# Performance work log

Measured on AMD Instinct MI355X. Metric: run time of the kernel, lower is better.

The kernel has to match this reference:

```python
import jax, jax.numpy as jnp
import numpy as np

STATE_DIM = 256
LATENT_DIM = 64
HIDDEN = 64
NUM_EMB = 2048
BATCH = 32768


def setup_inputs() -> dict:
    key = jax.random.key(0)
    ks = jax.random.split(key, 10)
    s = lambda *sh: 1.0 / np.sqrt(sh[0])
    return {
        "x": jax.random.normal(ks[0], (BATCH, STATE_DIM), dtype=jnp.float32),
        # encoder: Linear(state_dim, 64) -> ReLU -> Linear(64, latent_dim)
        "enc_w1": jax.random.uniform(ks[1], (STATE_DIM, HIDDEN), jnp.float32, -s(STATE_DIM), s(STATE_DIM)),
        "enc_b1": jax.random.uniform(ks[2], (HIDDEN,), jnp.float32, -s(STATE_DIM), s(STATE_DIM)),
        "enc_w2": jax.random.uniform(ks[3], (HIDDEN, LATENT_DIM), jnp.float32, -s(HIDDEN), s(HIDDEN)),
        "enc_b2": jax.random.uniform(ks[4], (LATENT_DIM,), jnp.float32, -s(HIDDEN), s(HIDDEN)),
        # codebook
        "emb": jax.random.normal(ks[5], (NUM_EMB, LATENT_DIM), dtype=jnp.float32),
        # decoder: Linear(latent_dim, 64) -> ReLU -> Linear(64, state_dim)
        "dec_w1": jax.random.uniform(ks[6], (LATENT_DIM, HIDDEN), jnp.float32, -s(LATENT_DIM), s(LATENT_DIM)),
        "dec_b1": jax.random.uniform(ks[7], (HIDDEN,), jnp.float32, -s(LATENT_DIM), s(LATENT_DIM)),
        "dec_w2": jax.random.uniform(ks[8], (HIDDEN, STATE_DIM), jnp.float32, -s(HIDDEN), s(HIDDEN)),
        "dec_b2": jax.random.uniform(ks[9], (STATE_DIM,), jnp.float32, -s(HIDDEN), s(HIDDEN)),
    }


def reference(x, enc_w1, enc_b1, enc_w2, enc_b2, emb, dec_w1, dec_b1, dec_w2, dec_b2):
    # encoder MLP: z_e [B, latent]
    h = jax.nn.relu(x @ enc_w1 + enc_b1)
    z_e = h @ enc_w2 + enc_b2
    # squared euclidean distances to codebook, expanded form: [B, K]
    # ||z - e||^2 = ||z||^2 - 2 z.e + ||e||^2  (same argmin as broadcast form)
    d = (jnp.sum(z_e * z_e, axis=1, keepdims=True)
         - 2.0 * (z_e @ emb.T)
         + jnp.sum(emb * emb, axis=1)[None, :])
    z_q_idx = jnp.argmin(d, axis=1)           # [B]
    z_q = emb[z_q_idx]                        # [B, latent]
    # decoder MLP
    hd = jax.nn.relu(z_q @ dec_w1 + dec_b1)
    x_recon = hd @ dec_w2 + dec_b2
    return (x_recon, z_e, z_q)
```

## Files before the change

### kernel.cpp

```cpp
#include <hip/hip_runtime.h>

#define BATCH   32768
#define SD      256
#define LD      64
#define HDIM    64
#define NEMB    2048
#define REFINE_THR_Q 5e-4f

typedef short  short8 __attribute__((ext_vector_type(8)));
typedef float  f32x4  __attribute__((ext_vector_type(4)));

__device__ __forceinline__ unsigned short f2bf(float f) {
    unsigned int u = __float_as_uint(f);
    u = (u + 0x7FFFu + ((u >> 16) & 1u)) >> 16;
    return (unsigned short)u;
}
__device__ __forceinline__ float bf2f(unsigned short h) {
    return __uint_as_float(((unsigned int)h) << 16);
}

__global__ __launch_bounds__(256) void k0_all(const float* __restrict__ emb,
                                              const float* __restrict__ dw1,
                                              const float* __restrict__ dw2,
                                              const float* __restrict__ ew1,
                                              const float* __restrict__ ew2,
                                              float* __restrict__ e2q,
                                              unsigned short* __restrict__ eh,
                                              unsigned short* __restrict__ el,
                                              unsigned short* __restrict__ w1h,
                                              unsigned short* __restrict__ w1l,
                                              unsigned short* __restrict__ w2h,
                                              unsigned short* __restrict__ w2l,
                                              unsigned short* __restrict__ w1eh,
                                              unsigned short* __restrict__ w1em,
                                              unsigned short* __restrict__ w1el,
                                              unsigned short* __restrict__ w2eh,
                                              unsigned short* __restrict__ w2em,
                                              unsigned short* __restrict__ w2el,
                                              int* __restrict__ count) {
    int b = blockIdx.x;
    int t = threadIdx.x;
    if (b < 8) {
        int k = b * 256 + t;
        if (k == 0) *count = 0;
        const float* er = emb + (size_t)k * LD;
        unsigned short hrow[LD], lrow[LD];
        float s = 0.f;
#pragma unroll
        for (int q = 0; q < LD; ++q) {
            float v = er[q];
            s += v * v;
            unsigned short h = f2bf(v);
            hrow[q] = h;
            lrow[q] = f2bf(v - bf2f(h));
        }
        e2q[k] = -0.5f * s;
        short8* dh = (short8*)(eh + (size_t)k * LD);
        short8* dl = (short8*)(el + (size_t)k * LD);
#pragma unroll
        for (int q = 0; q < 8; ++q) {
            dh[q] = *(short8*)&hrow[q * 8];
            dl[q] = *(short8*)&lrow[q * 8];
        }
    } else if (b < 24) {
        int e = (b - 8) * 256 + t;
        int j = e >> 6, k = e & 63;
        float v = dw1[k * HDIM + j];
        unsigned short h = f2bf(v);
        w1h[e] = h; w1l[e] = f2bf(v - bf2f(h));
    } else if (b < 88) {
        int e = (b - 24) * 256 + t;
        int j = e >> 6, k = e & 63;
        float v = dw2[k * SD + j];
        unsigned short h = f2bf(v);
        w2h[e] = h; w2l[e] = f2bf(v - bf2f(h));
    } else if (b < 152) {
        int e = (b - 88) * 256 + t;
        int kt = e >> 11, j = (e & 2047) >> 5, kk = e & 31;
        int k = kt * 32 + kk;
        float v = ew1[k * HDIM + j];
        unsigned short h = f2bf(v);
        float r1 = v - bf2f(h);
        unsigned short m = f2bf(r1);
        float r2 = r1 - bf2f(m);
        w1eh[e] = h; w1em[e] = m; w1el[e] = f2bf(r2);
    } else {
        int e = (b - 152) * 256 + t;
        int kt = e >> 11, j = (e & 2047) >> 5, kk = e & 31;
        int k = kt * 32 + kk;
        float v = ew2[k * LD + j];
        unsigned short h = f2bf(v);
        float r1 = v - bf2f(h);
        unsigned short m = f2bf(r1);
        float r2 = r1 - bf2f(m);
        w2eh[e] = h; w2em[e] = m; w2el[e] = f2bf(r2);
    }
}

#define MF(Afr, Bfr, C) __builtin_amdgcn_mfma_f32_16x16x32_bf16(Afr, Bfr, C, 0, 0, 0)

#define E_WLOAD(P, KT, JT) do {                                             \
    size_t wo_ = (size_t)(KT) * 2048 + ((JT) * 16 + lo) * 32 + hi * 8;      \
    P##h = *(const short8*)(w1eh + wo_);                                    \
    P##m = *(const short8*)(w1em + wo_);                                    \
    P##l = *(const short8*)(w1el + wo_);                                    \
} while (0)

#define E_COMP(P, JT) do {                                                  \
    f32x4 c_ = c1[JT];                                                      \
    c_ = MF(xl8, P##h, c_);                                                 \
    c_ = MF(xm8, P##m, c_);                                                 \
    c_ = MF(xh8, P##l, c_);                                                 \
    c_ = MF(xm8, P##h, c_);                                                 \
    c_ = MF(xh8, P##m, c_);                                                 \
    c_ = MF(xh8, P##h, c_);                                                 \
    c1[JT] = c_;                                                            \
} while (0)

#define K2_LOAD(P, t) do {                                                  \
    const unsigned short* ph_ = ehp + (size_t)(t) * 16 * LD;                \
    const unsigned short* pl_ = elp + (size_t)(t) * 16 * LD;                \
    P##a0 = *(const short8*)(ph_);                                          \
    P##a1 = *(const short8*)(ph_ + 32);                                     \
    P##a2 = *(const short8*)(pl_);                                          \
    P##a3 = *(const short8*)(pl_ + 32);                                     \
    P##e2 = *(const f32x4*)(e2q + cbase + (t) * 16 + hi * 4);               \
} while (0)

#define K2_COMP(P, t) do {                                                  \
    f32x4 acc_[4];                                                          \
    _Pragma("unroll")                                                       \
    for (int g = 0; g < 4; ++g) {                                           \
        f32x4 c_;                                                           \
        c_ = __builtin_amdgcn_mfma_f32_16x16x32_bf16(P##a0, bh[g][0], P##e2, 0, 0, 0); \
        c_ = __builtin_amdgcn_mfma_f32_16x16x32_bf16(P##a1, bh[g][1], c_, 0, 0, 0);    \
        c_ = __builtin_amdgcn_mfma_f32_16x16x32_bf16(P##a2, bh[g][0], c_, 0, 0, 0);    \
        c_ = __builtin_amdgcn_mfma_f32_16x16x32_bf16(P##a3, bh[g][1], c_, 0, 0, 0);    \
        c_ = __builtin_amdgcn_mfma_f32_16x16x32_bf16(P##a0, bl[g][0], c_, 0, 0, 0);    \
        c_ = __builtin_amdgcn_mfma_f32_16x16x32_bf16(P##a1, bl[g][1], c_, 0, 0, 0);    \
        acc_[g] = c_;                                                       \
    }                                                                       \
    _Pragma("unroll")                                                       \
    for (int g = 0; g < 4; ++g) {                                           \
        float m_ = fmaxf(fmaxf(acc_[g][0], acc_[g][1]),                     \
                         fmaxf(acc_[g][2], acc_[g][3]));                    \
        bool win_ = (m_ > bb[g]);                                           \
        qv[g] = win_ ? acc_[g] : qv[g];                                     \
        tt[g] = win_ ? (t) : tt[g];                                         \
        b2v[g] = fmaxf(b2v[g], fminf(bb[g], m_));                           \
        bb[g] = fmaxf(bb[g], m_);                                           \
    }                                                                       \
} while (0)

__global__ __launch_bounds__(256, 2) void k_fused(const float* __restrict__ x,
                                                  const unsigned short* __restrict__ w1eh,
                                                  const unsigned short* __restrict__ w1em,
                                                  const unsigned short* __restrict__ w1el,
                                                  const float* __restrict__ b1,
                                                  const unsigned short* __restrict__ w2eh,
                                                  const unsigned short* __restrict__ w2em,
                                                  const unsigned short* __restrict__ w2el,
                                                  const float* __restrict__ b2,
                                                  const unsigned short* __restrict__ eh,
                                                  const unsigned short* __restrict__ el,
                                                  const float* __restrict__ e2q,
                                                  float* __restrict__ zOut,
                                                  int* __restrict__ idx,
                                                  int* __restrict__ list,
                                                  int* __restrict__ count) {
    __shared__ float hds[4][16 * 68];
    unsigned short* zlsH = (unsigned short*)hds;
    unsigned short* zlsL = (unsigned short*)hds + 64 * 68;
    __shared__ float Lb[4][64];
    __shared__ float Ls[4][64];
    __shared__ int   Li[4][64];

    int tid  = threadIdx.x;
    int lane = tid & 63;
    int w    = tid >> 6;
    int lo   = lane & 15;
    int hi   = lane >> 4;
    int rb   = blockIdx.x * 64;
    int rbw  = rb + w * 16;
    int row  = rbw + lo;
    const float* xrow = x + (size_t)row * SD;

    f32x4 c1[4];
#pragma unroll
    for (int jt = 0; jt < 4; ++jt) {
        float bj = b1[jt * 16 + lo];
        f32x4 c = {bj, bj, bj, bj};
        c1[jt] = c;
    }

    short8 Ph, Pm, Pl, Qh, Qm, Ql, Rh, Rm, Rl, Sh, Sm, Sl;
    float4 xc0, xc1, xn0, xn1;
    xc0 = *(const float4*)(xrow + hi * 8);
    xc1 = *(const float4*)(xrow + hi * 8 + 4);
    E_WLOAD(P, 0, 0); E_WLOAD(Q, 0, 1); E_WLOAD(R, 0, 2); E_WLOAD(S, 0, 3);

#pragma unroll 1
    for (int kt = 0; kt < 8; ++kt) {
        int ktn = (kt + 1) & 7;
        xn0 = *(const float4*)(xrow + ktn * 32 + hi * 8);
        xn1 = *(const float4*)(xrow + ktn * 32 + hi * 8 + 4);

        float v[8] = {xc0.x, xc0.y, xc0.z, xc0.w, xc1.x, xc1.y, xc1.z, xc1.w};
        unsigned short sh[8], sm[8], sl[8];
#pragma unroll
        for (int q = 0; q < 8; ++q) {
            unsigned short h = f2bf(v[q]);
            float r1 = v[q] - bf2f(h);
            unsigned short m = f2bf(r1);
            float r2 = r1 - bf2f(m);
            sh[q] = h; sm[q] = m; sl[q] = f2bf(r2);
        }
        short8 xh8 = *(short8*)sh, xm8 = *(short8*)sm, xl8 = *(short8*)sl;

        E_COMP(P, 0); E_WLOAD(P, ktn, 0);
        E_COMP(Q, 1); E_WLOAD(Q, ktn, 1);
        E_COMP(R, 2); E_WLOAD(R, ktn, 2);
        E_COMP(S, 3); E_WLOAD(S, ktn, 3);
        xc0 = xn0; xc1 = xn1;
    }

#pragma unroll
    for (int jt = 0; jt < 4; ++jt)
#pragma unroll
        for (int r = 0; r < 4; ++r)
            hds[w][(hi * 4 + r) * 68 + jt * 16 + lo] = fmaxf(c1[jt][r], 0.f);
    __syncthreads();

    f32x4 c2[4];
#pragma unroll
    for (int jt = 0; jt < 4; ++jt) {
        float bj = b2[jt * 16 + lo];
        f32x4 c = {bj, bj, bj, bj};
        c2[jt] = c;
    }
#pragma unroll
    for (int kt = 0; kt < 2; ++kt) {
        float4 a4 = *(const float4*)&hds[w][lo * 68 + kt * 32 + hi * 8];
        float4 b4 = *(const float4*)&hds[w][lo * 68 + kt * 32 + hi * 8 + 4];
        float v[8] = {a4.x, a4.y, a4.z, a4.w, b4.x, b4.y, b4.z, b4.w};
        unsigned short sh[8], sm[8], sl[8];
#pragma unroll
        for (int q = 0; q < 8; ++q) {
            unsigned short h = f2bf(v[q]);
            float r1 = v[q] - bf2f(h);
            unsigned short m = f2bf(r1);
            float r2 = r1 - bf2f(m);
            sh[q] = h; sm[q] = m; sl[q] = f2bf(r2);
        }
        short8 ah = *(short8*)sh, am = *(short8*)sm, al = *(short8*)sl;
#pragma unroll
        for (int jt = 0; jt < 4; ++jt) {
            size_t wo = (size_t)kt * 2048 + (jt * 16 + lo) * 32 + hi * 8;
            short8 bh8 = *(const short8*)(w2eh + wo);
            short8 bm8 = *(const short8*)(w2em + wo);
            short8 bl8 = *(const short8*)(w2el + wo);
            f32x4 c = c2[jt];
            c = MF(al, bh8, c);
            c = MF(am, bm8, c);
            c = MF(ah, bl8, c);
            c = MF(am, bh8, c);
            c = MF(ah, bm8, c);
            c = MF(ah, bh8, c);
            c2[jt] = c;
        }
    }
    __syncthreads();

#pragma unroll
    for (int jt = 0; jt < 4; ++jt) {
#pragma unroll
        for (int r = 0; r < 4; ++r) {
            float z = c2[jt][r];
            int lrow = w * 16 + hi * 4 + r;
            int col  = jt * 16 + lo;
            zOut[(size_t)(rb + lrow) * LD + col] = z;
            unsigned short hb = f2bf(z);
            zlsH[lrow * 68 + col] = hb;
            zlsL[lrow * 68 + col] = f2bf(z - bf2f(hb));
        }
    }
    __syncthreads();

    short8 bh[4][2], bl[4][2];
#pragma unroll
    for (int g = 0; g < 4; ++g) {
        int lr = g * 16 + lo;
        bh[g][0] = *(const short8*)&zlsH[lr * 68 + hi * 8];
        bh[g][1] = *(const short8*)&zlsH[lr * 68 + 32 + hi * 8];
        bl[g][0] = *(const short8*)&zlsL[lr * 68 + hi * 8];
        bl[g][1] = *(const short8*)&zlsL[lr * 68 + 32 + hi * 8];
    }

    float bb[4], b2v[4];
    f32x4 qv[4];
    int   tt[4];
#pragma unroll
    for (int g = 0; g < 4; ++g) {
        bb[g] = -3.0e38f; b2v[g] = -3.0e38f; tt[g] = 0;
        qv[g][0] = qv[g][1] = qv[g][2] = qv[g][3] = -3.0e38f;
    }

    const int cbase = w * (NEMB / 4);
    const unsigned short* ehp = eh + (size_t)(cbase + lo) * LD + hi * 8;
    const unsigned short* elp = el + (size_t)(cbase + lo) * LD + hi * 8;

    short8 Aa0, Aa1, Aa2, Aa3; f32x4 Ae2;
    short8 Ba0, Ba1, Ba2, Ba3; f32x4 Be2;
    short8 Ca0, Ca1, Ca2, Ca3; f32x4 Ce2;

    K2_LOAD(A, 0);
    K2_LOAD(B, 1);
    K2_LOAD(C, 2);

    for (int tb = 0; tb < 27; tb += 3) {
        K2_COMP(A, tb);     K2_LOAD(A, tb + 3);
        K2_COMP(B, tb + 1); K2_LOAD(B, tb + 4);
        K2_COMP(C, tb + 2); K2_LOAD(C, tb + 5);
    }
    K2_COMP(A, 27); K2_LOAD(A, 30);
    K2_COMP(B, 28); K2_LOAD(B, 31);
    K2_COMP(C, 29);
    K2_COMP(A, 30);
    K2_COMP(B, 31);

    float ss[4];
    int   ii[4];
#pragma unroll
    for (int g = 0; g < 4; ++g) {
        float s0 = qv[g][0], s1 = qv[g][1], s2 = qv[g][2], s3 = qv[g][3];
        float M01 = fmaxf(s0, s1), L01 = fminf(s0, s1);
        float M23 = fmaxf(s2, s3), L23 = fminf(s2, s3);
        int   d01 = (s1 > s0) ? 1 : 0;
        int   d23 = (s3 > s2) ? 3 : 2;
        bool  cp  = (M23 > M01);
        float within2 = fmaxf(fminf(M01, M23), cp ? L23 : L01);
        int   dd  = cp ? d23 : d01;
        ii[g] = cbase + tt[g] * 16 + hi * 4 + dd;
        ss[g] = fmaxf(b2v[g], within2);
    }

#pragma unroll
    for (int off = 16; off <= 32; off <<= 1) {
#pragma unroll
        for (int g = 0; g < 4; ++g) {
            float ob = __shfl_xor(bb[g], off);
            float os = __shfl_xor(ss[g], off);
            int   oi = __shfl_xor(ii[g], off);
            ss[g] = fmaxf(fmaxf(fminf(bb[g], ob), os), ss[g]);
            ii[g] = (ob > bb[g]) ? oi : ii[g];
            bb[g] = fmaxf(bb[g], ob);
        }
    }

    if (lane < 16) {
#pragma unroll
        for (int g = 0; g < 4; ++g) {
            Lb[w][g * 16 + lane] = bb[g];
            Ls[w][g * 16 + lane] = ss[g];
            Li[w][g * 16 + lane] = ii[g];
        }
    }
    __syncthreads();

    if (tid < 64) {
        float B = Lb[0][tid], S = Ls[0][tid];
        int   I = Li[0][tid];
#pragma unroll
        for (int w2 = 1; w2 < 4; ++w2) {
            float ob = Lb[w2][tid], os = Ls[w2][tid];
            int   oi = Li[w2][tid];
            S = fmaxf(fmaxf(fminf(B, ob), os), S);
            I = (ob > B) ? oi : I;
            B = fmaxf(B, ob);
        }
        idx[rb + tid] = I;
        if (B - S < REFINE_THR_Q) {
            int p = atomicAdd(count, 1);
            list[p] = rb + tid;
        }
    }
}

__global__ __launch_bounds__(256) void k3_refine(const float* __restrict__ z,
                                                 const float* __restrict__ emb,
                                                 const int* __restrict__ count,
                                                 const int* __restrict__ list,
                                                 int* __restrict__ idx) {
    __shared__ double sv[256];
    __shared__ int    sx[256];
    int tid = threadIdx.x;
    int n = *count;
    for (int g = blockIdx.x; g < n; g += gridDim.x) {
        int row = list[g];
        const float4* zr4 = (const float4*)(z + (size_t)row * LD);
        float4 zv[16];
#pragma unroll
        for (int q = 0; q < 16; ++q) zv[q] = zr4[q];

        double best = 1.0e300;
        int bi = NEMB;
#pragma unroll 2
        for (int c = 0; c < 8; ++c) {
            int k = tid * 8 + c;
            const float4* er = (const float4*)(emb + (size_t)k * LD);
            double d0 = 0.0, d1 = 0.0, d2 = 0.0, d3 = 0.0;
#pragma unroll
            for (int q = 0; q < 16; ++q) {
                float4 e4 = er[q];
                double tx = (double)zv[q].x - (double)e4.x;
                double ty = (double)zv[q].y - (double)e4.y;
                double tz = (double)zv[q].z - (double)e4.z;
                double tw = (double)zv[q].w - (double)e4.w;
                d0 += tx * tx; d1 += ty * ty; d2 += tz * tz; d3 += tw * tw;
            }
            double d = (d0 + d1) + (d2 + d3);
            if (d < best) { best = d; bi = k; }
        }
        sv[tid] = best; sx[tid] = bi;
        __syncthreads();
        for (int s = 128; s > 0; s >>= 1) {
            if (tid < s) {
                if (sv[tid + s] < sv[tid] ||
                    (sv[tid + s] == sv[tid] && sx[tid + s] < sx[tid])) {
                    sv[tid] = sv[tid + s]; sx[tid] = sx[tid + s];
                }
            }
            __syncthreads();
        }
        if (tid == 0) idx[row] = sx[0];
        __syncthreads();
    }
}

__global__ __launch_bounds__(256, 2) void k_dec(const int* __restrict__ idx,
                                                const float* __restrict__ emb,
                                                const unsigned short* __restrict__ w1h,
                                                const unsigned short* __restrict__ w1l,
                                                const float* __restrict__ b1,
                                                const unsigned short* __restrict__ w2h,
                                                const unsigned short* __restrict__ w2l,
                                                const float* __restrict__ b2,
                                                float* __restrict__ xrec,
                                                float* __restrict__ zq) {
    __shared__ float hds[4][16 * 68];
    int tid  = threadIdx.x;
    int lane = tid & 63;
    int w    = tid >> 6;
    int lo   = lane & 15;
    int hi   = lane >> 4;
    int rb   = blockIdx.x * 64 + w * 16;
    int row  = rb + lo;
    int ix   = idx[row];

    short8 zah[2], zal[2];
    {
        const float* er  = emb + (size_t)ix * LD + hi * 8;
        float* zqr = zq + (size_t)row * LD + hi * 8;
#pragma unroll
        for (int kt = 0; kt < 2; ++kt) {
            float4 a = *(const float4*)(er + kt * 32);
            float4 b = *(const float4*)(er + kt * 32 + 4);
            *(float4*)(zqr + kt * 32) = a;
            *(float4*)(zqr + kt * 32 + 4) = b;
            float v[8] = {a.x, a.y, a.z, a.w, b.x, b.y, b.z, b.w};
            unsigned short hh[8], ll[8];
#pragma unroll
            for (int q = 0; q < 8; ++q) {
                unsigned short hb = f2bf(v[q]);
                hh[q] = hb;
                ll[q] = f2bf(v[q] - bf2f(hb));
            }
            zah[kt] = *(short8*)hh;
            zal[kt] = *(short8*)ll;
        }
    }

#pragma unroll
    for (int jt = 0; jt < 4; ++jt) {
        float bj = b1[jt * 16 + lo];
        f32x4 c = {bj, bj, bj, bj};
#pragma unroll
        for (int kt = 0; kt < 2; ++kt) {
            short8 bh8 = *(const short8*)(w1h + (jt * 16 + lo) * LD + kt * 32 + hi * 8);
            short8 bl8 = *(const short8*)(w1l + (jt * 16 + lo) * LD + kt * 32 + hi * 8);
            c = __builtin_amdgcn_mfma_f32_16x16x32_bf16(zah[kt], bh8, c, 0, 0, 0);
            c = __builtin_amdgcn_mfma_f32_16x16x32_bf16(zah[kt], bl8, c, 0, 0, 0);
            c = __builtin_amdgcn_mfma_f32_16x16x32_bf16(zal[kt], bh8, c, 0, 0, 0);
        }
#pragma unroll
        for (int r = 0; r < 4; ++r)
            hds[w][(hi * 4 + r) * 68 + jt * 16 + lo] = fmaxf(c[r], 0.f);
    }
    __syncthreads();

    short8 hah[2], hal[2];
#pragma unroll
    for (int kt = 0; kt < 2; ++kt) {
        float4 a = *(const float4*)&hds[w][lo * 68 + kt * 32 + hi * 8];
        float4 b = *(const float4*)&hds[w][lo * 68 + kt * 32 + hi * 8 + 4];
        float v[8] = {a.x, a.y, a.z, a.w, b.x, b.y, b.z, b.w};
        unsigned short hh[8], ll[8];
#pragma unroll
        for (int q = 0; q < 8; ++q) {
            unsigned short hb = f2bf(v[q]);
            hh[q] = hb;
            ll[q] = f2bf(v[q] - bf2f(hb));
        }
        hah[kt] = *(short8*)hh;
        hal[kt] = *(short8*)ll;
    }

    for (int jt = 0; jt < 16; ++jt) {
        float bj = b2[jt * 16 + lo];
        f32x4 c = {bj, bj, bj, bj};
#pragma unroll
        for (int kt = 0; kt < 2; ++kt) {
            short8 bh8 = *(const short8*)(w2h + (jt * 16 + lo) * LD + kt * 32 + hi * 8);
            short8 bl8 = *(const short8*)(w2l + (jt * 16 + lo) * LD + kt * 32 + hi * 8);
            c = __builtin_amdgcn_mfma_f32_16x16x32_bf16(hah[kt], bh8, c, 0, 0, 0);
            c = __builtin_amdgcn_mfma_f32_16x16x32_bf16(hah[kt], bl8, c, 0, 0, 0);
            c = __builtin_amdgcn_mfma_f32_16x16x32_bf16(hal[kt], bh8, c, 0, 0, 0);
        }
#pragma unroll
        for (int r = 0; r < 4; ++r)
            xrec[(size_t)(rb + hi * 4 + r) * SD + jt * 16 + lo] = c[r];
    }
}

extern "C" void kernel_launch(void* const* d_in, const int* in_sizes, int n_in,
                              void* d_out, int out_size, void* d_ws, size_t ws_size,
                              hipStream_t stream) {
    const float* x   = (const float*)d_in[0];
    const float* ew1 = (const float*)d_in[1];
    const float* eb1 = (const float*)d_in[2];
    const float* ew2 = (const float*)d_in[3];
    const float* eb2 = (const float*)d_in[4];
    const float* emb = (const float*)d_in[5];
    const float* dw1 = (const float*)d_in[6];
    const float* db1 = (const float*)d_in[7];
    const float* dw2 = (const float*)d_in[8];
    const float* db2 = (const float*)d_in[9];

    float* out  = (float*)d_out;
    float* xrec = out;
    float* zE   = out + (size_t)BATCH * SD;
    float* zQ   = zE + (size_t)BATCH * LD;

    char* xb = (char*)xrec;
    unsigned short* eh   = (unsigned short*)(xb + (8u << 20));
    unsigned short* el   = (unsigned short*)(xb + (8u << 20) + (NEMB * LD * 2));
    float*          e2q  = (float*)(xb + (9u << 20));
    unsigned short* w1eh = (unsigned short*)(xb + (10u << 20));
    unsigned short* w1em = w1eh + 16384;
    unsigned short* w1el = w1em + 16384;
    unsigned short* w2eh = w1el + 16384;
    unsigned short* w2em = w2eh + 4096;
    unsigned short* w2el = w2em + 4096;

    char* ws = (char*)d_ws;
    int*  count = (int*)ws;
    int*  idxA  = (int*)(ws + 16384);
    int*  list  = (int*)(ws + 147456);
    unsigned short* w1h = (unsigned short*)(ws + 278528);
    unsigned short* w1l = (unsigned short*)(ws + 286720);
    unsigned short* w2h = (unsigned short*)(ws + 294912);
    unsigned short* w2l = (unsigned short*)(ws + 327680);

    hipLaunchKernelGGL(k0_all,    dim3(168),        dim3(256), 0, stream,
                       emb, dw1, dw2, ew1, ew2, e2q, eh, el,
                       w1h, w1l, w2h, w2l, w1eh, w1em, w1el, w2eh, w2em, w2el, count);
    hipLaunchKernelGGL(k_fused,   dim3(BATCH / 64), dim3(256), 0, stream,
                       x, w1eh, w1em, w1el, eb1, w2eh, w2em, w2el, eb2,
                       eh, el, e2q, zE, idxA, list, count);
    hipLaunchKernelGGL(k3_refine, dim3(128),        dim3(256), 0, stream,
                       zE, emb, count, list, idxA);
    hipLaunchKernelGGL(k_dec,     dim3(BATCH / 64), dim3(256), 0, stream,
                       idxA, emb, w1h, w1l, db1, w2h, w2l, db2, xrec, zQ);
}
```

Measured before the change: 111.1 us.

## Fold fp64 argmin refinement into decoder kernel using per-row flags

Replaces the atomic-counter work list and the separate refine kernel with a per-row flag array written by the fused encoder/argmin kernel. The decoder kernel now scans its 64 rows' flags and, for each flagged row, runs the double-precision distance search across the whole block before decoding. This removes one kernel launch, the atomic append, and the count reset. The cost is that refinement work now sits inside decoder blocks, so blocks holding many near-tie rows can stall, and the decoder uses more shared memory and registers, which may reduce occupancy.

```diff
diff --git a/kernel.cpp b/kernel.cpp
--- a/kernel.cpp
+++ b/kernel.cpp
@@ -36,13 +36,11 @@
                                               unsigned short* __restrict__ w1el,
                                               unsigned short* __restrict__ w2eh,
                                               unsigned short* __restrict__ w2em,
-                                              unsigned short* __restrict__ w2el,
-                                              int* __restrict__ count) {
+                                              unsigned short* __restrict__ w2el) {
     int b = blockIdx.x;
     int t = threadIdx.x;
     if (b < 8) {
         int k = b * 256 + t;
-        if (k == 0) *count = 0;
         const float* er = emb + (size_t)k * LD;
         unsigned short hrow[LD], lrow[LD];
         float s = 0.f;
@@ -166,8 +164,7 @@
                                                   const float* __restrict__ e2q,
                                                   float* __restrict__ zOut,
                                                   int* __restrict__ idx,
-                                                  int* __restrict__ list,
-                                                  int* __restrict__ count) {
+                                                  int* __restrict__ flags) {
     __shared__ float hds[4][16 * 68];
     unsigned short* zlsH = (unsigned short*)hds;
     unsigned short* zlsL = (unsigned short*)hds + 64 * 68;
@@ -379,29 +376,44 @@
             B = fmaxf(B, ob);
         }
         idx[rb + tid] = I;
-        if (B - S < REFINE_THR_Q) {
-            int p = atomicAdd(count, 1);
-            list[p] = rb + tid;
-        }
+        flags[rb + tid] = (B - S < REFINE_THR_Q) ? 1 : 0;
     }
 }
 
-__global__ __launch_bounds__(256) void k3_refine(const float* __restrict__ z,
-                                                 const float* __restrict__ emb,
-                                                 const int* __restrict__ count,
-                                                 const int* __restrict__ list,
-                                                 int* __restrict__ idx) {
+__global__ __launch_bounds__(256, 2) void k_dec(const int* __restrict__ flags,
+                                                const float* __restrict__ zE,
+                                                int* __restrict__ idx,
+                                                const float* __restrict__ emb,
+                                                const unsigned short* __restrict__ w1h,
+                                                const unsigned short* __restrict__ w1l,
+                                                const float* __restrict__ b1,
+                                                const unsigned short* __restrict__ w2h,
+                                                const unsigned short* __restrict__ w2l,
+                                                const float* __restrict__ b2,
+                                                float* __restrict__ xrec,
+                                                float* __restrict__ zq) {
+    __shared__ float hds[4][16 * 68];
+    __shared__ int   flg[64];
     __shared__ double sv[256];
     __shared__ int    sx[256];
-    int tid = threadIdx.x;
-    int n = *count;
-    for (int g = blockIdx.x; g < n; g += gridDim.x) {
-        int row = list[g];
-        const float4* zr4 = (const float4*)(z + (size_t)row * LD);
+    int tid  = threadIdx.x;
+    int lane = tid & 63;
+    int w    = tid >> 6;
+    int lo   = lane & 15;
+    int hi   = lane >> 4;
+    int rb0  = blockIdx.x * 64;
+    int rb   = rb0 + w * 16;
+    int row  = rb + lo;
+
+    if (tid < 64) flg[tid] = flags[rb0 + tid];
+    __syncthreads();
+    for (int r = 0; r < 64; ++r) {
+        if (flg[r] == 0) continue;
+        int rrow = rb0 + r;
+        const float4* zr4 = (const float4*)(zE + (size_t)rrow * LD);
         float4 zv[16];
 #pragma unroll
         for (int q = 0; q < 16; ++q) zv[q] = zr4[q];
-
         double best = 1.0e300;
         int bi = NEMB;
 #pragma unroll 2
@@ -432,30 +444,11 @@
             }
             __syncthreads();
         }
-        if (tid == 0) idx[row] = sx[0];
+        if (tid == 0) idx[rrow] = sx[0];
         __syncthreads();
     }
-}
-
-__global__ __launch_bounds__(256, 2) void k_dec(const int* __restrict__ idx,
-                                                const float* __restrict__ emb,
-                                                const unsigned short* __restrict__ w1h,
-                                                const unsigned short* __restrict__ w1l,
-                                                const float* __restrict__ b1,
-                                                const unsigned short* __restrict__ w2h,
-                                                const unsigned short* __restrict__ w2l,
-                                                const float* __restrict__ b2,
-                                                float* __restrict__ xrec,
-                                                float* __restrict__ zq) {
-    __shared__ float hds[4][16 * 68];
-    int tid  = threadIdx.x;
-    int lane = tid & 63;
-    int w    = tid >> 6;
-    int lo   = lane & 15;
-    int hi   = lane >> 4;
-    int rb   = blockIdx.x * 64 + w * 16;
-    int row  = rb + lo;
-    int ix   = idx[row];
+
+    int ix = idx[row];
 
     short8 zah[2], zal[2];
     {
@@ -563,22 +556,19 @@
     unsigned short* w2el = w2em + 4096;
 
     char* ws = (char*)d_ws;
-    int*  count = (int*)ws;
     int*  idxA  = (int*)(ws + 16384);
-    int*  list  = (int*)(ws + 147456);
+    int*  flags = (int*)(ws + 147456);
     unsigned short* w1h = (unsigned short*)(ws + 278528);
     unsigned short* w1l = (unsigned short*)(ws + 286720);
     unsigned short* w2h = (unsigned short*)(ws + 294912);
     unsigned short* w2l = (unsigned short*)(ws + 327680);
 
-    hipLaunchKernelGGL(k0_all,    dim3(168),        dim3(256), 0, stream,
+    hipLaunchKernelGGL(k0_all,  dim3(168),        dim3(256), 0, stream,
                        emb, dw1, dw2, ew1, ew2, e2q, eh, el,
-                       w1h, w1l, w2h, w2l, w1eh, w1em, w1el, w2eh, w2em, w2el, count);
-    hipLaunchKernelGGL(k_fused,   dim3(BATCH / 64), dim3(256), 0, stream,
+                       w1h, w1l, w2h, w2l, w1eh, w1em, w1el, w2eh, w2em, w2el);
+    hipLaunchKernelGGL(k_fused, dim3(BATCH / 64), dim3(256), 0, stream,
                        x, w1eh, w1em, w1el, eb1, w2eh, w2em, w2el, eb2,
-                       eh, el, e2q, zE, idxA, list, count);
-    hipLaunchKernelGGL(k3_refine, dim3(128),        dim3(256), 0, stream,
-                       zE, emb, count, list, idxA);
-    hipLaunchKernelGGL(k_dec,     dim3(BATCH / 64), dim3(256), 0, stream,
-                       idxA, emb, w1h, w1l, db1, w2h, w2l, db2, xrec, zQ);
+                       eh, el, e2q, zE, idxA, flags);
+    hipLaunchKernelGGL(k_dec,   dim3(BATCH / 64), dim3(256), 0, stream,
+                       flags, zE, idxA, emb, w1h, w1l, db1, w2h, w2l, db2, xrec, zQ);
 }
```

Result: no change. 112.1 us (+0.9%).
